# Kernel optimization log

Measured on AMD Instinct MI355X. Metric: run time of the kernel, lower is better.

Reference implementation:

```python
import jax, jax.numpy as jnp
import numpy as np

MASK_FILL = -(2 ** 15)  # value used by the torch module's masked_fill


def setup_inputs() -> dict:
    key = jax.random.key(0)
    kq, kk, kv, km = jax.random.split(key, 4)
    B, H, S, D = 2, 16, 2048, 64
    Q = jax.random.normal(kq, (B, H, S, D), dtype=jnp.float32)
    K = jax.random.normal(kk, (B, H, S, D), dtype=jnp.float32)
    V = jax.random.normal(kv, (B, H, S, D), dtype=jnp.float32)
    mask = jax.random.randint(km, (B, 1, S, S), 0, 2, dtype=jnp.int32)
    return {"Q": Q, "K": K, "V": V, "mask": mask}


def reference(Q, K, V, mask):
    d_k = Q.shape[-1]
    # scores: [B,H,S,S]
    e = jnp.einsum('bhqd,bhkd->bhqk', Q, K) / jnp.sqrt(jnp.float32(d_k)).astype(Q.dtype)
    e = jnp.where(mask == 0, jnp.asarray(MASK_FILL, dtype=e.dtype), e)
    a = jax.nn.softmax(e, axis=-1)
    y = jnp.einsum('bhqk,bhkd->bhqd', a, V)
    return y
```

## Files before the change

kernel.cpp:

```cpp
#include <hip/hip_runtime.h>
#include <stdint.h>


#define SS 2048
#define DD 64
#define KT 64
#define NT 32
#define QB 64

#define KS0 0
#define VT0 8192
#define KS1 16384
#define VT1 24576
#define SMEM_SZ 32768

#define SCL2 0.18033688011112042f

typedef __attribute__((ext_vector_type(8))) short bf16x8;
typedef __attribute__((ext_vector_type(16))) float f32x16;

static __device__ __forceinline__ unsigned pk2(float f0, float f1) {
  unsigned r;
  asm("v_cvt_pk_bf16_f32 %0, %1, %2" : "=v"(r) : "v"(f0), "v"(f1));
  return r;
}

#define LSWAP(A, B) asm("v_permlane32_swap_b32 %0, %1" : "+v"(A), "+v"(B))

#define BAR() do {                              \
  asm volatile("" ::: "memory");                \
  __builtin_amdgcn_s_waitcnt(0xC07F);           \
  __builtin_amdgcn_s_barrier();                 \
  asm volatile("" ::: "memory");                \
} while (0)

#define MFMA32(A, B, C) __builtin_amdgcn_mfma_f32_32x32x16_bf16((A), (B), (C), 0, 0, 0)

__global__ __launch_bounds__(256, 2)
void attn_mfma(const float* __restrict__ Q, const float* __restrict__ K,
               const float* __restrict__ V, const int* __restrict__ mask,
               float* __restrict__ out) {
  __shared__ alignas(16) uint8_t smem[SMEM_SZ];

  const int tid = threadIdx.x;
  const int wv = tid >> 6;
  const int l = tid & 63;
  const int l31 = l & 31;
  const int h = l >> 5;
  const int x7 = l & 7;

  const int qg = wv & 1;
  const int kg = wv >> 1;

  const int bid = blockIdx.x;
  const int qblk = bid & 31;
  const int bh = bid >> 5;
  const int b = bh >> 4;
  const size_t base = (size_t)bh * SS * DD;
  const int qrow = qblk * QB + 32 * qg + l31;

  const int kr = tid >> 2;
  const int kq = tid & 3;
  const int va_ = tid >> 4;
  const int vc = tid & 15;
  const int vc1 = 4 * (vc & 1);
  const int vch = vc >> 1;
  const int vsub = 8 * (va_ & 1);
  const int vcq = va_ >> 1;
  const int gvx = x7 ^ (l31 >> 3);

  bf16x8 qf0, qf1, qf2, qf3;
  {
    const float* qp = Q + base + (size_t)qrow * DD + 8 * h;
    uint4 pk;
    float4 qa, qb;
    qa = *(const float4*)(qp);      qb = *(const float4*)(qp + 4);
    pk.x = pk2(qa.x * SCL2, qa.y * SCL2); pk.y = pk2(qa.z * SCL2, qa.w * SCL2);
    pk.z = pk2(qb.x * SCL2, qb.y * SCL2); pk.w = pk2(qb.z * SCL2, qb.w * SCL2);
    qf0 = __builtin_bit_cast(bf16x8, pk);
    qa = *(const float4*)(qp + 16); qb = *(const float4*)(qp + 20);
    pk.x = pk2(qa.x * SCL2, qa.y * SCL2); pk.y = pk2(qa.z * SCL2, qa.w * SCL2);
    pk.z = pk2(qb.x * SCL2, qb.y * SCL2); pk.w = pk2(qb.z * SCL2, qb.w * SCL2);
    qf1 = __builtin_bit_cast(bf16x8, pk);
    qa = *(const float4*)(qp + 32); qb = *(const float4*)(qp + 36);
    pk.x = pk2(qa.x * SCL2, qa.y * SCL2); pk.y = pk2(qa.z * SCL2, qa.w * SCL2);
    pk.z = pk2(qb.x * SCL2, qb.y * SCL2); pk.w = pk2(qb.z * SCL2, qb.w * SCL2);
    qf2 = __builtin_bit_cast(bf16x8, pk);
    qa = *(const float4*)(qp + 48); qb = *(const float4*)(qp + 52);
    pk.x = pk2(qa.x * SCL2, qa.y * SCL2); pk.y = pk2(qa.z * SCL2, qa.w * SCL2);
    pk.z = pk2(qb.x * SCL2, qb.y * SCL2); pk.w = pk2(qb.z * SCL2, qb.w * SCL2);
    qf3 = __builtin_bit_cast(bf16x8, pk);
  }

  f32x16 oacc0 = {0.f,0.f,0.f,0.f,0.f,0.f,0.f,0.f,0.f,0.f,0.f,0.f,0.f,0.f,0.f,0.f};
  f32x16 oacc1 = {0.f,0.f,0.f,0.f,0.f,0.f,0.f,0.f,0.f,0.f,0.f,0.f,0.f,0.f,0.f,0.f};
  float lrun = 0.f;

  float4 kL0, kL1, kL2, kL3, vL0, vL1, vL2, vL3;

#define LOADKV(T) do {                                                    \
    const float* kp_ = K + base + (size_t)((T)*KT + kr) * DD + kq * 16;   \
    kL0 = *(const float4*)(kp_);                                          \
    kL1 = *(const float4*)(kp_ + 4);                                      \
    kL2 = *(const float4*)(kp_ + 8);                                      \
    kL3 = *(const float4*)(kp_ + 12);                                     \
    const float* vp_ = V + base + (size_t)((T)*KT + 4 * va_) * DD + 4 * vc;\
    vL0 = *(const float4*)(vp_);                                          \
    vL1 = *(const float4*)(vp_ + DD);                                     \
    vL2 = *(const float4*)(vp_ + 2 * DD);                                 \
    vL3 = *(const float4*)(vp_ + 3 * DD);                                 \
  } while (0)

#define STAGE(KB, VB) do {                                                \
    uint4 c_;                                                             \
    c_.x = pk2(kL0.x, kL0.y); c_.y = pk2(kL0.z, kL0.w);                   \
    c_.z = pk2(kL1.x, kL1.y); c_.w = pk2(kL1.z, kL1.w);                   \
    *(uint4*)((KB) + kr * 128 + (((2 * kq) ^ (kr & 7)) << 4)) = c_;       \
    c_.x = pk2(kL2.x, kL2.y); c_.y = pk2(kL2.z, kL2.w);                   \
    c_.z = pk2(kL3.x, kL3.y); c_.w = pk2(kL3.z, kL3.w);                   \
    *(uint4*)((KB) + kr * 128 + (((2 * kq + 1) ^ (kr & 7)) << 4)) = c_;   \
    uint2 w_;                                                             \
    w_.x = pk2(vL0.x, vL1.x); w_.y = pk2(vL2.x, vL3.x);                   \
    *(uint2*)((VB) + (4*vc+0) * 128 + (((vcq ^ (vc1 + 0) ^ vch) << 4)) + vsub) = w_; \
    w_.x = pk2(vL0.y, vL1.y); w_.y = pk2(vL2.y, vL3.y);                   \
    *(uint2*)((VB) + (4*vc+1) * 128 + (((vcq ^ (vc1 + 1) ^ vch) << 4)) + vsub) = w_; \
    w_.x = pk2(vL0.z, vL1.z); w_.y = pk2(vL2.z, vL3.z);                   \
    *(uint2*)((VB) + (4*vc+2) * 128 + (((vcq ^ (vc1 + 2) ^ vch) << 4)) + vsub) = w_; \
    w_.x = pk2(vL0.w, vL1.w); w_.y = pk2(vL2.w, vL3.w);                   \
    *(uint2*)((VB) + (4*vc+3) * 128 + (((vcq ^ (vc1 + 3) ^ vch) << 4)) + vsub) = w_; \
  } while (0)

  LOADKV(0);
  STAGE(smem + KS0, smem + VT0);
  LOADKV(1);

  const int* mbase = mask + (size_t)b * SS * SS + (size_t)qrow * SS + 32 * kg + 4 * h;
  int4 mi0 = *(const int4*)(mbase + 0);
  int4 mi1 = *(const int4*)(mbase + 8);
  int4 mi2 = *(const int4*)(mbase + 16);
  int4 mi3 = *(const int4*)(mbase + 24);

  BAR();

  for (int t = 0; t < NT; ++t) {
    const int db = t & 1;
    uint8_t* kbc = smem + (db ? KS1 : KS0);
    uint8_t* vbc = smem + (db ? VT1 : VT0);
    uint8_t* kbn = smem + (db ? KS0 : KS1);
    uint8_t* vbn = smem + (db ? VT0 : VT1);

    STAGE(kbn, vbn);

    const int tp2 = (t + 2 < NT) ? (t + 2) : (NT - 1);
    LOADKV(tp2);
    const int tp1 = (t + 1 < NT) ? (t + 1) : (NT - 1);
    int4 mn0 = *(const int4*)(mbase + tp1 * KT + 0);
    int4 mn1 = *(const int4*)(mbase + tp1 * KT + 8);
    int4 mn2 = *(const int4*)(mbase + tp1 * KT + 16);
    int4 mn3 = *(const int4*)(mbase + tp1 * KT + 24);

    f32x16 sacc = {0.f,0.f,0.f,0.f,0.f,0.f,0.f,0.f,0.f,0.f,0.f,0.f,0.f,0.f,0.f,0.f};
    {
      const uint8_t* krow = kbc + (32 * kg + l31) * 128;
      bf16x8 kf0 = *(const bf16x8*)(krow + (((0 + h) ^ x7) << 4));
      bf16x8 kf1 = *(const bf16x8*)(krow + (((2 + h) ^ x7) << 4));
      bf16x8 kf2 = *(const bf16x8*)(krow + (((4 + h) ^ x7) << 4));
      bf16x8 kf3 = *(const bf16x8*)(krow + (((6 + h) ^ x7) << 4));
      sacc = MFMA32(kf0, qf0, sacc);
      sacc = MFMA32(kf1, qf1, sacc);
      sacc = MFMA32(kf2, qf2, sacc);
      sacc = MFMA32(kf3, qf3, sacc);
    }

    float p0  = (mi0.x != 0) ? __builtin_amdgcn_exp2f(sacc[0])  : 0.f;
    float p1  = (mi0.y != 0) ? __builtin_amdgcn_exp2f(sacc[1])  : 0.f;
    float p2  = (mi0.z != 0) ? __builtin_amdgcn_exp2f(sacc[2])  : 0.f;
    float p3  = (mi0.w != 0) ? __builtin_amdgcn_exp2f(sacc[3])  : 0.f;
    float p4  = (mi1.x != 0) ? __builtin_amdgcn_exp2f(sacc[4])  : 0.f;
    float p5  = (mi1.y != 0) ? __builtin_amdgcn_exp2f(sacc[5])  : 0.f;
    float p6  = (mi1.z != 0) ? __builtin_amdgcn_exp2f(sacc[6])  : 0.f;
    float p7  = (mi1.w != 0) ? __builtin_amdgcn_exp2f(sacc[7])  : 0.f;
    float p8  = (mi2.x != 0) ? __builtin_amdgcn_exp2f(sacc[8])  : 0.f;
    float p9  = (mi2.y != 0) ? __builtin_amdgcn_exp2f(sacc[9])  : 0.f;
    float p10 = (mi2.z != 0) ? __builtin_amdgcn_exp2f(sacc[10]) : 0.f;
    float p11 = (mi2.w != 0) ? __builtin_amdgcn_exp2f(sacc[11]) : 0.f;
    float p12 = (mi3.x != 0) ? __builtin_amdgcn_exp2f(sacc[12]) : 0.f;
    float p13 = (mi3.y != 0) ? __builtin_amdgcn_exp2f(sacc[13]) : 0.f;
    float p14 = (mi3.z != 0) ? __builtin_amdgcn_exp2f(sacc[14]) : 0.f;
    float p15 = (mi3.w != 0) ? __builtin_amdgcn_exp2f(sacc[15]) : 0.f;
    lrun += ((p0 + p1) + (p2 + p3)) + ((p4 + p5) + (p6 + p7)) +
            ((p8 + p9) + (p10 + p11)) + ((p12 + p13) + (p14 + p15));

    unsigned k0 = pk2(p0, p1),   k1 = pk2(p2, p3),
             k2 = pk2(p4, p5),   k3 = pk2(p6, p7),
             k4 = pk2(p8, p9),   k5 = pk2(p10, p11),
             k6 = pk2(p12, p13), k7 = pk2(p14, p15);
    uint4 bw;
    LSWAP(k0, k2);
    LSWAP(k1, k3);
    bw.x = k0; bw.y = k1; bw.z = k2; bw.w = k3;
    bf16x8 pB0 = __builtin_bit_cast(bf16x8, bw);
    LSWAP(k4, k6);
    LSWAP(k5, k7);
    bw.x = k4; bw.y = k5; bw.z = k6; bw.w = k7;
    bf16x8 pB1 = __builtin_bit_cast(bf16x8, bw);

    {
      const uint8_t* vrow0 = vbc + (l31) * 128;
      const uint8_t* vrow1 = vbc + (32 + l31) * 128;
      bf16x8 vf0 = *(const bf16x8*)(vrow0 + (((4 * kg + 0 + h) ^ gvx) << 4));
      bf16x8 vf1 = *(const bf16x8*)(vrow0 + (((4 * kg + 2 + h) ^ gvx) << 4));
      bf16x8 vf2 = *(const bf16x8*)(vrow1 + (((4 * kg + 0 + h) ^ gvx ^ 4) << 4));
      bf16x8 vf3 = *(const bf16x8*)(vrow1 + (((4 * kg + 2 + h) ^ gvx ^ 4) << 4));
      oacc0 = MFMA32(vf0, pB0, oacc0);
      oacc0 = MFMA32(vf1, pB1, oacc0);
      oacc1 = MFMA32(vf2, pB0, oacc1);
      oacc1 = MFMA32(vf3, pB1, oacc1);
    }

    mi0 = mn0; mi1 = mn1; mi2 = mn2; mi3 = mn3;

    BAR();
  }

  const float l32 = lrun + __shfl_xor(lrun, 32);

  float* xs = (float*)smem;
  const int xbase = qg * 2176 + l31 * 68;
  if (kg == 1) {
#pragma unroll
    for (int xq = 0; xq < 4; ++xq) {
      float4 o;
      o.x = oacc0[4*xq+0]; o.y = oacc0[4*xq+1]; o.z = oacc0[4*xq+2]; o.w = oacc0[4*xq+3];
      *(float4*)(xs + xbase + 8 * xq + 4 * h) = o;
      o.x = oacc1[4*xq+0]; o.y = oacc1[4*xq+1]; o.z = oacc1[4*xq+2]; o.w = oacc1[4*xq+3];
      *(float4*)(xs + xbase + 32 + 8 * xq + 4 * h) = o;
    }
    if (h == 0) xs[4352 + qg * 32 + l31] = l32;
  }
  BAR();
  if (kg == 0) {
    const float ltot = l32 + xs[4352 + qg * 32 + l31];
    const float inv = (ltot > 0.f) ? (1.f / ltot) : 0.f;
    float* orow = out + base + (size_t)qrow * DD;
#pragma unroll
    for (int xq = 0; xq < 4; ++xq) {
      float4 po = *(const float4*)(xs + xbase + 8 * xq + 4 * h);
      float4 o;
      o.x = (oacc0[4*xq+0] + po.x) * inv;
      o.y = (oacc0[4*xq+1] + po.y) * inv;
      o.z = (oacc0[4*xq+2] + po.z) * inv;
      o.w = (oacc0[4*xq+3] + po.w) * inv;
      *(float4*)(orow + 8 * xq + 4 * h) = o;
      po = *(const float4*)(xs + xbase + 32 + 8 * xq + 4 * h);
      o.x = (oacc1[4*xq+0] + po.x) * inv;
      o.y = (oacc1[4*xq+1] + po.y) * inv;
      o.z = (oacc1[4*xq+2] + po.z) * inv;
      o.w = (oacc1[4*xq+3] + po.w) * inv;
      *(float4*)(orow + 32 + 8 * xq + 4 * h) = o;
    }
  }
}

extern "C" void kernel_launch(void* const* d_in, const int* in_sizes, int n_in,
                              void* d_out, int out_size, void* d_ws, size_t ws_size,
                              hipStream_t stream) {
  (void)in_sizes; (void)n_in; (void)out_size; (void)d_ws; (void)ws_size;
  const float* Q = (const float*)d_in[0];
  const float* K = (const float*)d_in[1];
  const float* V = (const float*)d_in[2];
  const int* mask = (const int*)d_in[3];
  float* out = (float*)d_out;
  attn_mfma<<<1024, 256, 0, stream>>>(Q, K, V, mask, out);
}
```

Measured before the change: 210.2 us.

## Software-pipeline PV MFMA one tile behind QK with triple-buffered V

Restructures the KV loop so the P·V MFMAs for tile t-1 are issued at the start of iteration t, alongside the QK^T MFMAs for tile t, with the final P·V drained after the loop. V shared memory goes from double to triple buffering (LDS grows from 32KB to 40KB) so the previous V tile stays valid while the next is staged. The staging store is also moved after the QK MFMAs and skipped on the last iteration. The aim is to overlap the MFMA pipe with the exp/convert softmax work and hide the latency between them, at the cost of more LDS and extra live registers for the carried P fragments.

```diff
diff --git a/kernel.cpp b/kernel.cpp
--- a/kernel.cpp
+++ b/kernel.cpp
@@ -9,10 +9,11 @@
 #define QB 64
 
 #define KS0 0
-#define VT0 8192
-#define KS1 16384
+#define KS1 8192
+#define VT0 16384
 #define VT1 24576
-#define SMEM_SZ 32768
+#define VT2 32768
+#define SMEM_SZ 40960
 
 #define SCL2 0.18033688011112042f
 
@@ -140,28 +141,33 @@
   int4 mi2 = *(const int4*)(mbase + 16);
   int4 mi3 = *(const int4*)(mbase + 24);
 
+  uint8_t* kbC = smem + KS0;
+  uint8_t* kbN = smem + KS1;
+  uint8_t* vbP = smem + VT2;
+  uint8_t* vbC = smem + VT0;
+  uint8_t* vbN = smem + VT1;
+
+  bf16x8 pB0p = {0,0,0,0,0,0,0,0}, pB1p = {0,0,0,0,0,0,0,0};
+
   BAR();
 
   for (int t = 0; t < NT; ++t) {
-    const int db = t & 1;
-    uint8_t* kbc = smem + (db ? KS1 : KS0);
-    uint8_t* vbc = smem + (db ? VT1 : VT0);
-    uint8_t* kbn = smem + (db ? KS0 : KS1);
-    uint8_t* vbn = smem + (db ? VT0 : VT1);
-
-    STAGE(kbn, vbn);
-
-    const int tp2 = (t + 2 < NT) ? (t + 2) : (NT - 1);
-    LOADKV(tp2);
-    const int tp1 = (t + 1 < NT) ? (t + 1) : (NT - 1);
-    int4 mn0 = *(const int4*)(mbase + tp1 * KT + 0);
-    int4 mn1 = *(const int4*)(mbase + tp1 * KT + 8);
-    int4 mn2 = *(const int4*)(mbase + tp1 * KT + 16);
-    int4 mn3 = *(const int4*)(mbase + tp1 * KT + 24);
+    if (t > 0) {
+      const uint8_t* vrow0 = vbP + (l31) * 128;
+      const uint8_t* vrow1 = vbP + (32 + l31) * 128;
+      bf16x8 vf0 = *(const bf16x8*)(vrow0 + (((4 * kg + 0 + h) ^ gvx) << 4));
+      bf16x8 vf1 = *(const bf16x8*)(vrow0 + (((4 * kg + 2 + h) ^ gvx) << 4));
+      bf16x8 vf2 = *(const bf16x8*)(vrow1 + (((4 * kg + 0 + h) ^ gvx ^ 4) << 4));
+      bf16x8 vf3 = *(const bf16x8*)(vrow1 + (((4 * kg + 2 + h) ^ gvx ^ 4) << 4));
+      oacc0 = MFMA32(vf0, pB0p, oacc0);
+      oacc0 = MFMA32(vf1, pB1p, oacc0);
+      oacc1 = MFMA32(vf2, pB0p, oacc1);
+      oacc1 = MFMA32(vf3, pB1p, oacc1);
+    }
 
     f32x16 sacc = {0.f,0.f,0.f,0.f,0.f,0.f,0.f,0.f,0.f,0.f,0.f,0.f,0.f,0.f,0.f,0.f};
     {
-      const uint8_t* krow = kbc + (32 * kg + l31) * 128;
+      const uint8_t* krow = kbC + (32 * kg + l31) * 128;
       bf16x8 kf0 = *(const bf16x8*)(krow + (((0 + h) ^ x7) << 4));
       bf16x8 kf1 = *(const bf16x8*)(krow + (((2 + h) ^ x7) << 4));
       bf16x8 kf2 = *(const bf16x8*)(krow + (((4 + h) ^ x7) << 4));
@@ -171,6 +177,16 @@
       sacc = MFMA32(kf2, qf2, sacc);
       sacc = MFMA32(kf3, qf3, sacc);
     }
+
+    if (t + 1 < NT) STAGE(kbN, vbN);
+
+    const int tp2 = (t + 2 < NT) ? (t + 2) : (NT - 1);
+    LOADKV(tp2);
+    const int tp1 = (t + 1 < NT) ? (t + 1) : (NT - 1);
+    int4 mn0 = *(const int4*)(mbase + tp1 * KT + 0);
+    int4 mn1 = *(const int4*)(mbase + tp1 * KT + 8);
+    int4 mn2 = *(const int4*)(mbase + tp1 * KT + 16);
+    int4 mn3 = *(const int4*)(mbase + tp1 * KT + 24);
 
     float p0  = (mi0.x != 0) ? __builtin_amdgcn_exp2f(sacc[0])  : 0.f;
     float p1  = (mi0.y != 0) ? __builtin_amdgcn_exp2f(sacc[1])  : 0.f;
@@ -199,28 +215,30 @@
     LSWAP(k0, k2);
     LSWAP(k1, k3);
     bw.x = k0; bw.y = k1; bw.z = k2; bw.w = k3;
-    bf16x8 pB0 = __builtin_bit_cast(bf16x8, bw);
+    pB0p = __builtin_bit_cast(bf16x8, bw);
     LSWAP(k4, k6);
     LSWAP(k5, k7);
     bw.x = k4; bw.y = k5; bw.z = k6; bw.w = k7;
-    bf16x8 pB1 = __builtin_bit_cast(bf16x8, bw);
-
-    {
-      const uint8_t* vrow0 = vbc + (l31) * 128;
-      const uint8_t* vrow1 = vbc + (32 + l31) * 128;
-      bf16x8 vf0 = *(const bf16x8*)(vrow0 + (((4 * kg + 0 + h) ^ gvx) << 4));
-      bf16x8 vf1 = *(const bf16x8*)(vrow0 + (((4 * kg + 2 + h) ^ gvx) << 4));
-      bf16x8 vf2 = *(const bf16x8*)(vrow1 + (((4 * kg + 0 + h) ^ gvx ^ 4) << 4));
-      bf16x8 vf3 = *(const bf16x8*)(vrow1 + (((4 * kg + 2 + h) ^ gvx ^ 4) << 4));
-      oacc0 = MFMA32(vf0, pB0, oacc0);
-      oacc0 = MFMA32(vf1, pB1, oacc0);
-      oacc1 = MFMA32(vf2, pB0, oacc1);
-      oacc1 = MFMA32(vf3, pB1, oacc1);
-    }
+    pB1p = __builtin_bit_cast(bf16x8, bw);
 
     mi0 = mn0; mi1 = mn1; mi2 = mn2; mi3 = mn3;
 
+    uint8_t* kt_ = kbC; kbC = kbN; kbN = kt_;
+    uint8_t* vt_ = vbP; vbP = vbC; vbC = vbN; vbN = vt_;
     BAR();
+  }
+
+  {
+    const uint8_t* vrow0 = vbP + (l31) * 128;
+    const uint8_t* vrow1 = vbP + (32 + l31) * 128;
+    bf16x8 vf0 = *(const bf16x8*)(vrow0 + (((4 * kg + 0 + h) ^ gvx) << 4));
+    bf16x8 vf1 = *(const bf16x8*)(vrow0 + (((4 * kg + 2 + h) ^ gvx) << 4));
+    bf16x8 vf2 = *(const bf16x8*)(vrow1 + (((4 * kg + 0 + h) ^ gvx ^ 4) << 4));
+    bf16x8 vf3 = *(const bf16x8*)(vrow1 + (((4 * kg + 2 + h) ^ gvx ^ 4) << 4));
+    oacc0 = MFMA32(vf0, pB0p, oacc0);
+    oacc0 = MFMA32(vf1, pB1p, oacc0);
+    oacc1 = MFMA32(vf2, pB0p, oacc1);
+    oacc1 = MFMA32(vf3, pB1p, oacc1);
   }
 
   const float l32 = lrun + __shfl_xor(lrun, 32);
```

Result: no change. 210.0 us (-0.1%).

## Prepack mask tile into LDS bitmask via ballot and coalesce K loads

Applied to the files above, without the earlier changes.

Before the main loop, each block reads its full 64x2048 int32 mask slab with fully coalesced row loads and compresses it into a per-tile bitmask in shared memory using wavefront ballots. The loop then reads one 32-bit word per lane instead of four int4 global loads per iteration. K staging is changed to row-strided float4 loads for better coalescing, and LDS grows to hold the bitmask. The cost is a serial prologue that fetches the whole mask slab before any compute starts, plus higher LDS use that may reduce occupancy.

```diff
diff --git a/kernel.cpp b/kernel.cpp
--- a/kernel.cpp
+++ b/kernel.cpp
@@ -9,10 +9,11 @@
 #define QB 64
 
 #define KS0 0
-#define VT0 8192
-#define KS1 16384
+#define KS1 8192
+#define VT0 16384
 #define VT1 24576
-#define SMEM_SZ 32768
+#define BITS 32768
+#define SMEM_SZ 49152
 
 #define SCL2 0.18033688011112042f
 
@@ -59,8 +60,11 @@
   const size_t base = (size_t)bh * SS * DD;
   const int qrow = qblk * QB + 32 * qg + l31;
 
-  const int kr = tid >> 2;
-  const int kq = tid & 3;
+  const int krw = tid >> 4;
+  const int kc = tid & 15;
+  const int kch = kc >> 1;
+  const int ksb = 8 * (kc & 1);
+  const int kxr = krw & 7;
   const int va_ = tid >> 4;
   const int vc = tid & 15;
   const int vc1 = 4 * (vc & 1);
@@ -92,6 +96,21 @@
     qf3 = __builtin_bit_cast(bf16x8, pk);
   }
 
+  {
+    uint32_t* bits = (uint32_t*)(smem + BITS);
+    const int* mrow = mask + (size_t)b * SS * SS + (size_t)(qblk * QB) * SS;
+    for (int R = wv; R < 2048; R += 4) {
+      const int q = R >> 5;
+      const int jp = R & 31;
+      const int m = mrow[(size_t)q * SS + 64 * jp + l];
+      const unsigned long long bal = __ballot(m != 0);
+      if (l == 0) {
+        bits[(2 * jp) * 64 + q] = (uint32_t)bal;
+        bits[(2 * jp + 1) * 64 + q] = (uint32_t)(bal >> 32);
+      }
+    }
+  }
+
   f32x16 oacc0 = {0.f,0.f,0.f,0.f,0.f,0.f,0.f,0.f,0.f,0.f,0.f,0.f,0.f,0.f,0.f,0.f};
   f32x16 oacc1 = {0.f,0.f,0.f,0.f,0.f,0.f,0.f,0.f,0.f,0.f,0.f,0.f,0.f,0.f,0.f,0.f};
   float lrun = 0.f;
@@ -99,11 +118,11 @@
   float4 kL0, kL1, kL2, kL3, vL0, vL1, vL2, vL3;
 
 #define LOADKV(T) do {                                                    \
-    const float* kp_ = K + base + (size_t)((T)*KT + kr) * DD + kq * 16;   \
+    const float* kp_ = K + base + (size_t)((T)*KT + krw) * DD + 4 * kc;   \
     kL0 = *(const float4*)(kp_);                                          \
-    kL1 = *(const float4*)(kp_ + 4);                                      \
-    kL2 = *(const float4*)(kp_ + 8);                                      \
-    kL3 = *(const float4*)(kp_ + 12);                                     \
+    kL1 = *(const float4*)(kp_ + 16 * DD);                                \
+    kL2 = *(const float4*)(kp_ + 32 * DD);                                \
+    kL3 = *(const float4*)(kp_ + 48 * DD);                                \
     const float* vp_ = V + base + (size_t)((T)*KT + 4 * va_) * DD + 4 * vc;\
     vL0 = *(const float4*)(vp_);                                          \
     vL1 = *(const float4*)(vp_ + DD);                                     \
@@ -112,14 +131,15 @@
   } while (0)
 
 #define STAGE(KB, VB) do {                                                \
-    uint4 c_;                                                             \
-    c_.x = pk2(kL0.x, kL0.y); c_.y = pk2(kL0.z, kL0.w);                   \
-    c_.z = pk2(kL1.x, kL1.y); c_.w = pk2(kL1.z, kL1.w);                   \
-    *(uint4*)((KB) + kr * 128 + (((2 * kq) ^ (kr & 7)) << 4)) = c_;       \
-    c_.x = pk2(kL2.x, kL2.y); c_.y = pk2(kL2.z, kL2.w);                   \
-    c_.z = pk2(kL3.x, kL3.y); c_.w = pk2(kL3.z, kL3.w);                   \
-    *(uint4*)((KB) + kr * 128 + (((2 * kq + 1) ^ (kr & 7)) << 4)) = c_;   \
     uint2 w_;                                                             \
+    w_.x = pk2(kL0.x, kL0.y); w_.y = pk2(kL0.z, kL0.w);                   \
+    *(uint2*)((KB) + (krw) * 128 + (((kch ^ kxr) << 4) + ksb)) = w_;      \
+    w_.x = pk2(kL1.x, kL1.y); w_.y = pk2(kL1.z, kL1.w);                   \
+    *(uint2*)((KB) + (krw + 16) * 128 + (((kch ^ kxr) << 4) + ksb)) = w_; \
+    w_.x = pk2(kL2.x, kL2.y); w_.y = pk2(kL2.z, kL2.w);                   \
+    *(uint2*)((KB) + (krw + 32) * 128 + (((kch ^ kxr) << 4) + ksb)) = w_; \
+    w_.x = pk2(kL3.x, kL3.y); w_.y = pk2(kL3.z, kL3.w);                   \
+    *(uint2*)((KB) + (krw + 48) * 128 + (((kch ^ kxr) << 4) + ksb)) = w_; \
     w_.x = pk2(vL0.x, vL1.x); w_.y = pk2(vL2.x, vL3.x);                   \
     *(uint2*)((VB) + (4*vc+0) * 128 + (((vcq ^ (vc1 + 0) ^ vch) << 4)) + vsub) = w_; \
     w_.x = pk2(vL0.y, vL1.y); w_.y = pk2(vL2.y, vL3.y);                   \
@@ -134,12 +154,6 @@
   STAGE(smem + KS0, smem + VT0);
   LOADKV(1);
 
-  const int* mbase = mask + (size_t)b * SS * SS + (size_t)qrow * SS + 32 * kg + 4 * h;
-  int4 mi0 = *(const int4*)(mbase + 0);
-  int4 mi1 = *(const int4*)(mbase + 8);
-  int4 mi2 = *(const int4*)(mbase + 16);
-  int4 mi3 = *(const int4*)(mbase + 24);
-
   BAR();
 
   for (int t = 0; t < NT; ++t) {
@@ -153,11 +167,13 @@
 
     const int tp2 = (t + 2 < NT) ? (t + 2) : (NT - 1);
     LOADKV(tp2);
-    const int tp1 = (t + 1 < NT) ? (t + 1) : (NT - 1);
-    int4 mn0 = *(const int4*)(mbase + tp1 * KT + 0);
-    int4 mn1 = *(const int4*)(mbase + tp1 * KT + 8);
-    int4 mn2 = *(const int4*)(mbase + tp1 * KT + 16);
-    int4 mn3 = *(const int4*)(mbase + tp1 * KT + 24);
+
+    const uint32_t m32 =
+        *((const uint32_t*)(smem + BITS) + (2 * t + kg) * 64 + 32 * qg + l31);
+    const uint32_t n0 = (m32 >> (4 * h)) & 0xFu;
+    const uint32_t n1 = (m32 >> (8 + 4 * h)) & 0xFu;
+    const uint32_t n2 = (m32 >> (16 + 4 * h)) & 0xFu;
+    const uint32_t n3 = (m32 >> (24 + 4 * h)) & 0xFu;
 
     f32x16 sacc = {0.f,0.f,0.f,0.f,0.f,0.f,0.f,0.f,0.f,0.f,0.f,0.f,0.f,0.f,0.f,0.f};
     {
@@ -172,22 +188,22 @@
       sacc = MFMA32(kf3, qf3, sacc);
     }
 
-    float p0  = (mi0.x != 0) ? __builtin_amdgcn_exp2f(sacc[0])  : 0.f;
-    float p1  = (mi0.y != 0) ? __builtin_amdgcn_exp2f(sacc[1])  : 0.f;
-    float p2  = (mi0.z != 0) ? __builtin_amdgcn_exp2f(sacc[2])  : 0.f;
-    float p3  = (mi0.w != 0) ? __builtin_amdgcn_exp2f(sacc[3])  : 0.f;
-    float p4  = (mi1.x != 0) ? __builtin_amdgcn_exp2f(sacc[4])  : 0.f;
-    float p5  = (mi1.y != 0) ? __builtin_amdgcn_exp2f(sacc[5])  : 0.f;
-    float p6  = (mi1.z != 0) ? __builtin_amdgcn_exp2f(sacc[6])  : 0.f;
-    float p7  = (mi1.w != 0) ? __builtin_amdgcn_exp2f(sacc[7])  : 0.f;
-    float p8  = (mi2.x != 0) ? __builtin_amdgcn_exp2f(sacc[8])  : 0.f;
-    float p9  = (mi2.y != 0) ? __builtin_amdgcn_exp2f(sacc[9])  : 0.f;
-    float p10 = (mi2.z != 0) ? __builtin_amdgcn_exp2f(sacc[10]) : 0.f;
-    float p11 = (mi2.w != 0) ? __builtin_amdgcn_exp2f(sacc[11]) : 0.f;
-    float p12 = (mi3.x != 0) ? __builtin_amdgcn_exp2f(sacc[12]) : 0.f;
-    float p13 = (mi3.y != 0) ? __builtin_amdgcn_exp2f(sacc[13]) : 0.f;
-    float p14 = (mi3.z != 0) ? __builtin_amdgcn_exp2f(sacc[14]) : 0.f;
-    float p15 = (mi3.w != 0) ? __builtin_amdgcn_exp2f(sacc[15]) : 0.f;
+    float p0  = (n0 & 1u) ? __builtin_amdgcn_exp2f(sacc[0])  : 0.f;
+    float p1  = (n0 & 2u) ? __builtin_amdgcn_exp2f(sacc[1])  : 0.f;
+    float p2  = (n0 & 4u) ? __builtin_amdgcn_exp2f(sacc[2])  : 0.f;
+    float p3  = (n0 & 8u) ? __builtin_amdgcn_exp2f(sacc[3])  : 0.f;
+    float p4  = (n1 & 1u) ? __builtin_amdgcn_exp2f(sacc[4])  : 0.f;
+    float p5  = (n1 & 2u) ? __builtin_amdgcn_exp2f(sacc[5])  : 0.f;
+    float p6  = (n1 & 4u) ? __builtin_amdgcn_exp2f(sacc[6])  : 0.f;
+    float p7  = (n1 & 8u) ? __builtin_amdgcn_exp2f(sacc[7])  : 0.f;
+    float p8  = (n2 & 1u) ? __builtin_amdgcn_exp2f(sacc[8])  : 0.f;
+    float p9  = (n2 & 2u) ? __builtin_amdgcn_exp2f(sacc[9])  : 0.f;
+    float p10 = (n2 & 4u) ? __builtin_amdgcn_exp2f(sacc[10]) : 0.f;
+    float p11 = (n2 & 8u) ? __builtin_amdgcn_exp2f(sacc[11]) : 0.f;
+    float p12 = (n3 & 1u) ? __builtin_amdgcn_exp2f(sacc[12]) : 0.f;
+    float p13 = (n3 & 2u) ? __builtin_amdgcn_exp2f(sacc[13]) : 0.f;
+    float p14 = (n3 & 4u) ? __builtin_amdgcn_exp2f(sacc[14]) : 0.f;
+    float p15 = (n3 & 8u) ? __builtin_amdgcn_exp2f(sacc[15]) : 0.f;
     lrun += ((p0 + p1) + (p2 + p3)) + ((p4 + p5) + (p6 + p7)) +
             ((p8 + p9) + (p10 + p11)) + ((p12 + p13) + (p14 + p15));
 
@@ -217,8 +233,6 @@
       oacc1 = MFMA32(vf2, pB0, oacc1);
       oacc1 = MFMA32(vf3, pB1, oacc1);
     }
-
-    mi0 = mn0; mi1 = mn1; mi2 = mn2; mi3 = mn3;
 
     BAR();
   }
```

Result: slower. 460.0 us (+118.8%).
